# Optimization experiments

Hardware: AMD Instinct MI355X
Metric: run time of the kernel (lower is better)

The kernel has to match this reference:

```python
import jax, jax.numpy as jnp
import numpy as np

B, T, DIM, H, HD, K = 4, 2048, 1024, 16, 64, 4
QK = H * HD          # 1024
VD = 2 * H * HD      # 2048
EPS = 1e-5


def zrms(x, g):
    # zero-centered RMS norm with learned scale
    x = x - jnp.mean(x, axis=-1, keepdims=True)
    return x * jax.lax.rsqrt(jnp.mean(x * x, axis=-1, keepdims=True) + EPS) * g


def causal_dwconv(x, w):
    # x: [B,T,C], w: [K,1,C] (keras depthwise Conv1D kernel, groups=C)
    k = w.shape[0]
    return jax.lax.conv_general_dilated(
        x, w, window_strides=(1,), padding=[(k - 1, 0)],
        dimension_numbers=('NWC', 'WIO', 'NWC'),
        feature_group_count=x.shape[-1])


def setup_inputs() -> dict:
    key = jax.random.key(0)
    ks = jax.random.split(key, 12)
    s = lambda *sh: 1.0 / np.sqrt(sh[0])
    return {
        'x':  jax.random.normal(ks[0], (B, T, DIM), jnp.float32),
        'Wq': jax.random.normal(ks[1], (DIM, QK), jnp.float32) * s(DIM),
        'Wk': jax.random.normal(ks[2], (DIM, QK), jnp.float32) * s(DIM),
        'Wv': jax.random.normal(ks[3], (DIM, VD), jnp.float32) * s(DIM),
        'gq': jnp.ones((QK,), jnp.float32),
        'gk': jnp.ones((QK,), jnp.float32),
        'gv': jnp.ones((VD,), jnp.float32),
        'cq': jax.random.normal(ks[4], (K, 1, QK), jnp.float32) * 0.5,
        'ck': jax.random.normal(ks[5], (K, 1, QK), jnp.float32) * 0.5,
        'cv': jax.random.normal(ks[6], (K, 1, VD), jnp.float32) * 0.5,
        'Wa': jax.random.normal(ks[7], (DIM, H), jnp.float32) * s(DIM),
        'Wb': jax.random.normal(ks[8], (DIM, H), jnp.float32) * s(DIM),
        'Wo': jax.random.normal(ks[9], (VD, DIM), jnp.float32) * s(VD),
        'Wg': jax.random.normal(ks[10], (DIM, DIM), jnp.float32) * s(DIM),
    }


def reference(x, Wq, Wk, Wv, gq, gk, gv, cq, ck, cv, Wa, Wb, Wo, Wg):
    # 1) projections  2) zero-centered RMSNorm  3) causal depthwise conv (+silu)
    q = jax.nn.silu(causal_dwconv(zrms(x @ Wq, gq), cq))   # [B,T,QK]
    k = jax.nn.silu(causal_dwconv(zrms(x @ Wk, gk), ck))   # [B,T,QK]
    v = jax.nn.silu(causal_dwconv(zrms(x @ Wv, gv), cv))   # [B,T,VD]

    q = q.reshape(B, T, H, HD)
    k = k.reshape(B, T, H, HD)
    v = v.reshape(B, T, H, 2 * HD)

    # 4) per-head gating params
    alpha = jax.nn.sigmoid(x @ Wa)  # [B,T,H]
    beta = jax.nn.sigmoid(x @ Wb)   # [B,T,H]

    # 5) gated delta-rule recurrence over time (state S: [B,H,2*HD,HD])
    def step(S, inp):
        qt, kt, vt, at, bt = inp  # [B,H,HD],[B,H,HD],[B,H,2HD],[B,H],[B,H]
        a = at[..., None, None]
        upd = S + bt[..., None, None] * jnp.einsum('bhv,bhk->bhvk', vt, kt)
        S = a * upd + (1.0 - a) * S
        o = jnp.einsum('bhvk,bhk->bhv', S, qt)  # Q_t readout
        return S, o

    S0 = jnp.zeros((B, H, 2 * HD, HD), x.dtype)
    xs = (q.transpose(1, 0, 2, 3), k.transpose(1, 0, 2, 3),
          v.transpose(1, 0, 2, 3), alpha.transpose(1, 0, 2),
          beta.transpose(1, 0, 2))
    _, o = jax.lax.scan(step, S0, xs)          # o: [T,B,H,2HD]
    o = o.transpose(1, 0, 2, 3).reshape(B, T, VD)

    # 6) output projection + sigmoid output gate
    proj = o @ Wo                              # [B,T,DIM]
    return jax.nn.sigmoid(proj @ Wg) * proj
```

## Files before the change

### kernel.cpp

```cpp
#include <hip/hip_runtime.h>
#include <hip/hip_bf16.h>
#include <math.h>

#define RTOT 8192
#define TSEQ 2048

typedef __attribute__((ext_vector_type(8))) short short8;
typedef __attribute__((ext_vector_type(4))) float f32x4;
typedef unsigned short u16;
typedef unsigned int u32;

union U16x8 { uint4 v; u16 s[8]; };

__device__ __forceinline__ float sigmoidf_(float x) { return 1.f / (1.f + expf(-x)); }
__device__ __forceinline__ float bf2f(u16 v) { u32 u = ((u32)v) << 16; float f; __builtin_memcpy(&f, &u, 4); return f; }
__device__ __forceinline__ u16 f2bf(float f) {
  u32 u; __builtin_memcpy(&u, &f, 4);
  u32 r = (u + 0x7FFFu + ((u >> 16) & 1u)) >> 16;
  return (u16)r;
}
__device__ __forceinline__ void split2(float x, u16& h, u16& l) {
  u16 hh = f2bf(x);
  float hf = bf2f(hh);
  h = hh; l = f2bf(x - hf);
}

typedef const void __attribute__((address_space(1))) gvoid_t;
typedef void __attribute__((address_space(3))) lvoid_t;
__device__ __forceinline__ void gload_lds16(const void* g, void* l) {
  __builtin_amdgcn_global_load_lds((gvoid_t*)g, (lvoid_t*)l, 16, 0, 0);
}

template<int EPI>
__global__ __launch_bounds__(256) void gemm_sp(const u16* __restrict__ Ah, const u16* __restrict__ Al,
                                               const u16* __restrict__ Bh, const u16* __restrict__ Bl,
                                               float* __restrict__ Cf, u16* __restrict__ Ph,
                                               u16* __restrict__ Pl, const float* __restrict__ Pin,
                                               int M, int N, int K) {
  __shared__ u16 Ash[128 * 32], Asl[128 * 32];
  __shared__ u16 Bsh[128 * 32], Bsl[128 * 32];
  const int tid = threadIdx.x;
  const int l = tid & 63, w = tid >> 6;
  const int m0 = blockIdx.y * 128, n0 = blockIdx.x * 128;
  const int wr = w >> 1, wc = w & 1;
  f32x4 acc[4][4] = {};
  const int srow = (w << 5) + (l >> 2);
  const int scol = (l & 3) << 3;
  const size_t gA = (size_t)(m0 + srow) * K + scol;
  const size_t gB = (size_t)(n0 + srow) * K + scol;
  const int lo0 = (w * 2 + 0) * 512, lo1 = (w * 2 + 1) * 512;
  const int arow = wr * 64 + (l & 15), brow = wc * 64 + (l & 15);
  const int koff = 8 * (l >> 4);
  for (int k0 = 0; k0 < K; k0 += 32) {
    gload_lds16(Ah + gA + k0, &Ash[lo0]);
    gload_lds16(Ah + gA + 16 * K + k0, &Ash[lo1]);
    gload_lds16(Al + gA + k0, &Asl[lo0]);
    gload_lds16(Al + gA + 16 * K + k0, &Asl[lo1]);
    gload_lds16(Bh + gB + k0, &Bsh[lo0]);
    gload_lds16(Bh + gB + 16 * K + k0, &Bsh[lo1]);
    gload_lds16(Bl + gB + k0, &Bsl[lo0]);
    gload_lds16(Bl + gB + 16 * K + k0, &Bsl[lo1]);
    __syncthreads();
    short8 afh[4], afl[4], bfh[4], bfl[4];
#pragma unroll
    for (int m = 0; m < 4; ++m) {
      afh[m] = *(const short8*)&Ash[(arow + m * 16) * 32 + koff];
      afl[m] = *(const short8*)&Asl[(arow + m * 16) * 32 + koff];
    }
#pragma unroll
    for (int n = 0; n < 4; ++n) {
      bfh[n] = *(const short8*)&Bsh[(brow + n * 16) * 32 + koff];
      bfl[n] = *(const short8*)&Bsl[(brow + n * 16) * 32 + koff];
    }
#pragma unroll
    for (int m = 0; m < 4; ++m)
#pragma unroll
      for (int n = 0; n < 4; ++n) {
        acc[m][n] = __builtin_amdgcn_mfma_f32_16x16x32_bf16(afh[m], bfh[n], acc[m][n], 0, 0, 0);
        acc[m][n] = __builtin_amdgcn_mfma_f32_16x16x32_bf16(afh[m], bfl[n], acc[m][n], 0, 0, 0);
        acc[m][n] = __builtin_amdgcn_mfma_f32_16x16x32_bf16(afl[m], bfh[n], acc[m][n], 0, 0, 0);
      }
    __syncthreads();
  }
  const int rbase = m0 + wr * 64 + 4 * (l >> 4);
  const int cbase = n0 + wc * 64 + (l & 15);
#pragma unroll
  for (int m = 0; m < 4; ++m)
#pragma unroll
    for (int n = 0; n < 4; ++n)
#pragma unroll
      for (int r = 0; r < 4; ++r) {
        size_t idx = (size_t)(rbase + m * 16 + r) * N + (cbase + n * 16);
        float v = acc[m][n][r];
        if (EPI == 0) {
          Cf[idx] = v;
        } else if (EPI == 1) {
          Cf[idx] = v;
          u16 h, lo; split2(v, h, lo);
          Ph[idx] = h; Pl[idx] = lo;
        } else {
          Cf[idx] = Pin[idx] * sigmoidf_(v);
        }
      }
}

__global__ __launch_bounds__(256) void transcast_sp(const float* __restrict__ W,
                                                    u16* __restrict__ Wth, u16* __restrict__ Wtl,
                                                    int K, int N) {
  __shared__ float t[32][33];
  const int n0 = blockIdx.x * 32, k0 = blockIdx.y * 32;
  const int c = threadIdx.x & 31, rq = threadIdx.x >> 5;
#pragma unroll
  for (int i = 0; i < 4; ++i) t[rq * 4 + i][c] = W[(size_t)(k0 + rq * 4 + i) * N + n0 + c];
  __syncthreads();
#pragma unroll
  for (int i = 0; i < 4; ++i) {
    float v = t[c][rq * 4 + i];
    u16 h, lo; split2(v, h, lo);
    size_t idx = (size_t)(n0 + rq * 4 + i) * K + k0 + c;
    Wth[idx] = h; Wtl[idx] = lo;
  }
}

__global__ __launch_bounds__(256) void castx_sp(const float* __restrict__ x,
                                                u16* __restrict__ xh, u16* __restrict__ xl) {
  size_t i = (size_t)blockIdx.x * 256 + threadIdx.x;
  float4 v = ((const float4*)x)[i];
  ushort4 hh, ll;
  split2(v.x, hh.x, ll.x); split2(v.y, hh.y, ll.y);
  split2(v.z, hh.z, ll.z); split2(v.w, hh.w, ll.w);
  ((ushort4*)xh)[i] = hh; ((ushort4*)xl)[i] = ll;
}

template<int C>
__global__ __launch_bounds__(256) void zrms_kernel(const float* __restrict__ in,
                                                   const float* __restrict__ g,
                                                   float* __restrict__ out) {
  constexpr int NQ = C / 1024;
  __shared__ float red[4];
  const int tid = threadIdx.x;
  const size_t row = blockIdx.x;
  const float* x = in + row * C;
  float4 v[NQ];
  float s = 0.f;
#pragma unroll
  for (int i = 0; i < NQ; ++i) {
    v[i] = *(const float4*)(x + tid*4 + i*1024);
    s += v[i].x + v[i].y + v[i].z + v[i].w;
  }
#pragma unroll
  for (int o = 32; o > 0; o >>= 1) s += __shfl_xor(s, o, 64);
  if ((tid & 63) == 0) red[tid >> 6] = s;
  __syncthreads();
  const float mean = (red[0]+red[1]+red[2]+red[3]) * (1.f / C);
  __syncthreads();
  float ss = 0.f;
#pragma unroll
  for (int i = 0; i < NQ; ++i) {
    v[i].x -= mean; v[i].y -= mean; v[i].z -= mean; v[i].w -= mean;
    ss += v[i].x*v[i].x + v[i].y*v[i].y + v[i].z*v[i].z + v[i].w*v[i].w;
  }
#pragma unroll
  for (int o = 32; o > 0; o >>= 1) ss += __shfl_xor(ss, o, 64);
  if ((tid & 63) == 0) red[tid >> 6] = ss;
  __syncthreads();
  const float r = rsqrtf((red[0]+red[1]+red[2]+red[3]) * (1.f / C) + 1e-5f);
  float* y = out + row * C;
#pragma unroll
  for (int i = 0; i < NQ; ++i) {
    float4 g4 = *(const float4*)(g + tid*4 + i*1024);
    float4 o4;
    o4.x = v[i].x * r * g4.x;
    o4.y = v[i].y * r * g4.y;
    o4.z = v[i].z * r * g4.z;
    o4.w = v[i].w * r * g4.w;
    *(float4*)(y + tid*4 + i*1024) = o4;
  }
}

template<int C, int GSCALE>
__global__ __launch_bounds__(256) void conv_sp(const float* __restrict__ zn,
                                               const float* __restrict__ w,
                                               const float* __restrict__ g,
                                               u16* __restrict__ oh,
                                               u16* __restrict__ ol) {
  const size_t idx = (size_t)blockIdx.x * 256 + threadIdx.x;
  const int c = (int)(idx % (C/4)) * 4;
  const int row = (int)(idx / (C/4));
  const int t = row % TSEQ;
  float4 acc = {0.f, 0.f, 0.f, 0.f};
#pragma unroll
  for (int d = 0; d < 4; ++d) {
    if (t - d >= 0) {
      float4 xv = *(const float4*)(zn + (size_t)(row - d) * C + c);
      float4 wv = *(const float4*)(w + (size_t)(3 - d) * C + c);
      acc.x = fmaf(xv.x, wv.x, acc.x);
      acc.y = fmaf(xv.y, wv.y, acc.y);
      acc.z = fmaf(xv.z, wv.z, acc.z);
      acc.w = fmaf(xv.w, wv.w, acc.w);
    }
  }
  float a0 = acc.x * sigmoidf_(acc.x);
  float a1 = acc.y * sigmoidf_(acc.y);
  float a2 = acc.z * sigmoidf_(acc.z);
  float a3 = acc.w * sigmoidf_(acc.w);
  if (GSCALE) {
    float gv = g[(size_t)row * 16 + (c >> 7)];
    a0 *= gv; a1 *= gv; a2 *= gv; a3 *= gv;
  }
  ushort4 hh, ll;
  split2(a0, hh.x, ll.x); split2(a1, hh.y, ll.y);
  split2(a2, hh.z, ll.z); split2(a3, hh.w, ll.w);
  *(ushort4*)(oh + (size_t)row * C + c) = hh;
  *(ushort4*)(ol + (size_t)row * C + c) = ll;
}

__global__ __launch_bounds__(256) void gab_kernel(const float* __restrict__ x,
                                                  const float* __restrict__ Wa,
                                                  const float* __restrict__ Wb,
                                                  float* __restrict__ gout) {
  __shared__ float xs[1024];
  __shared__ float partial[256];
  const int tid = threadIdx.x;
  const size_t row = blockIdx.x;
  *(float4*)(&xs[tid*4]) = *(const float4*)(x + row*1024 + tid*4);
  __syncthreads();
  const int h = tid & 31;
  const int seg = tid >> 5;
  const float* W = (h < 16) ? Wa : Wb;
  const int col = h & 15;
  float s = 0.f;
  const int k0 = seg * 128;
  for (int k = 0; k < 128; ++k) s = fmaf(xs[k0 + k], W[(size_t)(k0 + k) * 16 + col], s);
  partial[tid] = s;
  __syncthreads();
  if (tid < 32) {
    float t2 = 0.f;
#pragma unroll
    for (int j = 0; j < 8; ++j) t2 += partial[j*32 + tid];
    partial[tid] = t2;
  }
  __syncthreads();
  if (tid < 16)
    gout[row*16 + tid] = sigmoidf_(partial[tid]) * sigmoidf_(partial[tid + 16]);
}

__global__ __launch_bounds__(256) void scan_kernel(const u16* __restrict__ kh,
                                                   const u16* __restrict__ kl,
                                                   const u16* __restrict__ vgh,
                                                   const u16* __restrict__ vgl,
                                                   u16* __restrict__ Sph,
                                                   u16* __restrict__ Spl) {
  __shared__ float Ks[64][68];
  __shared__ float Vs[64][36];
  const int tid = threadIdx.x;
  const int bid = blockIdx.x;
  const int vq = bid & 3, h = (bid >> 2) & 15, b = bid >> 6;
  const size_t rb = (size_t)b * TSEQ;
  const int vd_t = tid >> 3, kd0 = (tid & 7) * 8;
  float S[8] = {};
  const int sr = tid >> 2;
  const int kc0 = (tid & 3) * 16;
  const int vc0 = (tid & 3) * 8;
  for (int c = 0; c < 32; ++c) {
    {
      size_t off = (rb + (size_t)c * 64 + sr) * 1024 + h * 64 + kc0;
      U16x8 a0, a1, b0, b1;
      a0.v = *(const uint4*)(kh + off);     a1.v = *(const uint4*)(kh + off + 8);
      b0.v = *(const uint4*)(kl + off);     b1.v = *(const uint4*)(kl + off + 8);
#pragma unroll
      for (int j = 0; j < 8; ++j) {
        Ks[sr][kc0 + j]     = bf2f(a0.s[j]) + bf2f(b0.s[j]);
        Ks[sr][kc0 + 8 + j] = bf2f(a1.s[j]) + bf2f(b1.s[j]);
      }
      size_t voff = (rb + (size_t)c * 64 + sr) * 2048 + h * 128 + vq * 32 + vc0;
      U16x8 va, vb;
      va.v = *(const uint4*)(vgh + voff);   vb.v = *(const uint4*)(vgl + voff);
#pragma unroll
      for (int j = 0; j < 8; ++j) Vs[sr][vc0 + j] = bf2f(va.s[j]) + bf2f(vb.s[j]);
    }
    {
      size_t spc = (((size_t)(b * 16 + h) * 32) + c) * 8192 + (size_t)(vq * 32 + vd_t) * 64 + kd0;
      ushort4 h0, h1, l0, l1;
      split2(S[0], h0.x, l0.x); split2(S[1], h0.y, l0.y);
      split2(S[2], h0.z, l0.z); split2(S[3], h0.w, l0.w);
      split2(S[4], h1.x, l1.x); split2(S[5], h1.y, l1.y);
      split2(S[6], h1.z, l1.z); split2(S[7], h1.w, l1.w);
      *(ushort4*)(Sph + spc)     = h0;  *(ushort4*)(Sph + spc + 4) = h1;
      *(ushort4*)(Spl + spc)     = l0;  *(ushort4*)(Spl + spc + 4) = l1;
    }
    __syncthreads();
    for (int s = 0; s < 64; ++s) {
      float vv = Vs[s][vd_t];
      float k0v[4], k1v[4];
      *(float4*)k0v = *(const float4*)&Ks[s][kd0];
      *(float4*)k1v = *(const float4*)&Ks[s][kd0 + 4];
#pragma unroll
      for (int j = 0; j < 4; ++j) S[j] = fmaf(vv, k0v[j], S[j]);
#pragma unroll
      for (int j = 0; j < 4; ++j) S[4 + j] = fmaf(vv, k1v[j], S[4 + j]);
    }
    __syncthreads();
  }
}

__global__ __launch_bounds__(256) void pass2_sp(const u16* __restrict__ qh,
                                                const u16* __restrict__ ql,
                                                const u16* __restrict__ kh,
                                                const u16* __restrict__ vgh,
                                                const u16* __restrict__ Sph,
                                                const u16* __restrict__ Spl,
                                                u16* __restrict__ oh,
                                                u16* __restrict__ ol) {
  __shared__ u16 Qsh[64 * 72];
  __shared__ u16 Qsl[64 * 72];
  __shared__ u16 Ksm[64 * 72];
  __shared__ u16 Am[64 * 72];
  __shared__ u16 Vth[128 * 72];
  const int tid = threadIdx.x;
  const int l = tid & 63, w = tid >> 6;
  const int bid = blockIdx.x;
  const int c = bid & 31, h = (bid >> 5) & 15, b = bid >> 9;
  const size_t rb = (size_t)b * TSEQ + c * 64;
  const int fr = l & 15, fq = l >> 4;
  {
    int r = tid >> 2, c0 = (tid & 3) * 16;
    size_t off = (rb + r) * 1024 + h * 64 + c0;
    *(uint4*)&Qsh[r * 72 + c0]     = *(const uint4*)(qh + off);
    *(uint4*)&Qsh[r * 72 + c0 + 8] = *(const uint4*)(qh + off + 8);
    *(uint4*)&Qsl[r * 72 + c0]     = *(const uint4*)(ql + off);
    *(uint4*)&Qsl[r * 72 + c0 + 8] = *(const uint4*)(ql + off + 8);
    *(uint4*)&Ksm[r * 72 + c0]     = *(const uint4*)(kh + off);
    *(uint4*)&Ksm[r * 72 + c0 + 8] = *(const uint4*)(kh + off + 8);
  }
  {
    int s = tid >> 2, vd0 = (tid & 3) * 32;
    size_t off = (rb + s) * 2048 + h * 128 + vd0;
#pragma unroll
    for (int m4 = 0; m4 < 4; ++m4) {
      U16x8 r_; r_.v = *(const uint4*)(vgh + off + m4 * 8);
#pragma unroll
      for (int j = 0; j < 8; ++j) Vth[(vd0 + m4 * 8 + j) * 72 + s] = r_.s[j];
    }
  }
  __syncthreads();
  short8 aqh[2], aql[2];
#pragma unroll
  for (int kk = 0; kk < 2; ++kk) {
    aqh[kk] = *(const short8*)&Qsh[(w * 16 + fr) * 72 + kk * 32 + 8 * fq];
    aql[kk] = *(const short8*)&Qsl[(w * 16 + fr) * 72 + kk * 32 + 8 * fq];
  }
  f32x4 accA[4] = {};
#pragma unroll
  for (int n = 0; n < 4; ++n)
#pragma unroll
    for (int kk = 0; kk < 2; ++kk) {
      short8 bk = *(const short8*)&Ksm[(n * 16 + fr) * 72 + kk * 32 + 8 * fq];
      accA[n] = __builtin_amdgcn_mfma_f32_16x16x32_bf16(aqh[kk], bk, accA[n], 0, 0, 0);
    }
#pragma unroll
  for (int n = 0; n < 4; ++n)
#pragma unroll
    for (int rr = 0; rr < 4; ++rr) {
      int tt = w * 16 + 4 * fq + rr;
      int s = n * 16 + fr;
      Am[tt * 72 + s] = f2bf((s <= tt) ? accA[n][rr] : 0.f);
    }
  __syncthreads();
  f32x4 acc[8] = {};
#pragma unroll
  for (int kk = 0; kk < 2; ++kk) {
    short8 aa = *(const short8*)&Am[(w * 16 + fr) * 72 + kk * 32 + 8 * fq];
#pragma unroll
    for (int n = 0; n < 8; ++n) {
      short8 bv = *(const short8*)&Vth[(n * 16 + fr) * 72 + kk * 32 + 8 * fq];
      acc[n] = __builtin_amdgcn_mfma_f32_16x16x32_bf16(aa, bv, acc[n], 0, 0, 0);
    }
  }
  const size_t spb = (((size_t)(b * 16 + h) * 32) + c) * 8192;
#pragma unroll
  for (int n = 0; n < 8; ++n)
#pragma unroll
    for (int kk = 0; kk < 2; ++kk) {
      size_t soff = spb + (size_t)(n * 16 + fr) * 64 + kk * 32 + 8 * fq;
      short8 bh_ = *(const short8*)(Sph + soff);
      short8 bl_ = *(const short8*)(Spl + soff);
      acc[n] = __builtin_amdgcn_mfma_f32_16x16x32_bf16(aqh[kk], bh_, acc[n], 0, 0, 0);
      acc[n] = __builtin_amdgcn_mfma_f32_16x16x32_bf16(aqh[kk], bl_, acc[n], 0, 0, 0);
      acc[n] = __builtin_amdgcn_mfma_f32_16x16x32_bf16(aql[kk], bh_, acc[n], 0, 0, 0);
    }
#pragma unroll
  for (int n = 0; n < 8; ++n)
#pragma unroll
    for (int rr = 0; rr < 4; ++rr) {
      int tt = w * 16 + 4 * fq + rr;
      int vd = n * 16 + fr;
      u16 hh, ll;
      split2(acc[n][rr], hh, ll);
      size_t off = (rb + tt) * 2048 + h * 128 + vd;
      oh[off] = hh; ol[off] = ll;
    }
}

extern "C" void kernel_launch(void* const* d_in, const int* in_sizes, int n_in,
                              void* d_out, int out_size, void* d_ws, size_t ws_size,
                              hipStream_t stream) {
  (void)in_sizes; (void)n_in; (void)out_size; (void)ws_size;
  const float* x  = (const float*)d_in[0];
  const float* Wq = (const float*)d_in[1];
  const float* Wk = (const float*)d_in[2];
  const float* Wv = (const float*)d_in[3];
  const float* gq = (const float*)d_in[4];
  const float* gk = (const float*)d_in[5];
  const float* gv = (const float*)d_in[6];
  const float* cq = (const float*)d_in[7];
  const float* ck = (const float*)d_in[8];
  const float* cv = (const float*)d_in[9];
  const float* Wa = (const float*)d_in[10];
  const float* Wb = (const float*)d_in[11];
  const float* Wo = (const float*)d_in[12];
  const float* Wg = (const float*)d_in[13];
  float* out = (float*)d_out;
  char* ws = (char*)d_ws;

  const size_t MiB = 1024 * 1024;
  u16* Wq_h = (u16*)(ws + 0 * MiB);
  u16* Wq_l = (u16*)(ws + 2 * MiB);
  u16* Wk_h = (u16*)(ws + 4 * MiB);
  u16* Wk_l = (u16*)(ws + 6 * MiB);
  u16* Wv_h = (u16*)(ws + 8 * MiB);
  u16* Wv_l = (u16*)(ws + 12 * MiB);
  u16* Wo_h = (u16*)(ws + 16 * MiB);
  u16* Wo_l = (u16*)(ws + 20 * MiB);
  u16* Wg_h = (u16*)(ws + 24 * MiB);
  u16* Wg_l = (u16*)(ws + 26 * MiB);
  float* gbuf  = (float*)(ws + 28 * MiB);
  u16* x_h  = (u16*)(ws + 32 * MiB);
  u16* x_l  = (u16*)(ws + 48 * MiB);
  float* q_pre = (float*)(ws + 64 * MiB);
  float* k_pre = (float*)(ws + 96 * MiB);
  float* v_pre = (float*)(ws + 128 * MiB);
  u16* q_h = (u16*)(ws + 32 * MiB);
  u16* q_l = (u16*)(ws + 48 * MiB);
  u16* k_h = (u16*)(ws + 64 * MiB);
  u16* k_l = (u16*)(ws + 80 * MiB);
  u16* vg_h = (u16*)(ws + 96 * MiB);
  u16* vg_l = (u16*)d_out;
  u16* Sp_h = (u16*)(ws + 128 * MiB);
  u16* Sp_l = (u16*)(ws + 160 * MiB);
  u16* o_h  = (u16*)(ws + 192 * MiB);
  u16* o_l  = (u16*)d_out;
  float* proj = (float*)(ws + 64 * MiB);
  u16* p_h  = (u16*)(ws + 96 * MiB);
  u16* p_l  = (u16*)(ws + 112 * MiB);

  dim3 blk(256);
  castx_sp<<<dim3(8192), blk, 0, stream>>>(x, x_h, x_l);
  transcast_sp<<<dim3(32, 32), blk, 0, stream>>>(Wq, Wq_h, Wq_l, 1024, 1024);
  transcast_sp<<<dim3(32, 32), blk, 0, stream>>>(Wk, Wk_h, Wk_l, 1024, 1024);
  transcast_sp<<<dim3(64, 32), blk, 0, stream>>>(Wv, Wv_h, Wv_l, 1024, 2048);
  transcast_sp<<<dim3(32, 64), blk, 0, stream>>>(Wo, Wo_h, Wo_l, 2048, 1024);
  transcast_sp<<<dim3(32, 32), blk, 0, stream>>>(Wg, Wg_h, Wg_l, 1024, 1024);
  gab_kernel<<<dim3(8192), blk, 0, stream>>>(x, Wa, Wb, gbuf);
  gemm_sp<0><<<dim3(8, 64), blk, 0, stream>>>(x_h, x_l, Wq_h, Wq_l, q_pre, nullptr, nullptr, nullptr, 8192, 1024, 1024);
  gemm_sp<0><<<dim3(8, 64), blk, 0, stream>>>(x_h, x_l, Wk_h, Wk_l, k_pre, nullptr, nullptr, nullptr, 8192, 1024, 1024);
  gemm_sp<0><<<dim3(16, 64), blk, 0, stream>>>(x_h, x_l, Wv_h, Wv_l, v_pre, nullptr, nullptr, nullptr, 8192, 2048, 1024);
  zrms_kernel<1024><<<dim3(8192), blk, 0, stream>>>(q_pre, gq, q_pre);
  zrms_kernel<1024><<<dim3(8192), blk, 0, stream>>>(k_pre, gk, k_pre);
  zrms_kernel<2048><<<dim3(8192), blk, 0, stream>>>(v_pre, gv, v_pre);
  conv_sp<1024, 0><<<dim3(8192), blk, 0, stream>>>(q_pre, cq, nullptr, q_h, q_l);
  conv_sp<1024, 0><<<dim3(8192), blk, 0, stream>>>(k_pre, ck, nullptr, k_h, k_l);
  conv_sp<2048, 1><<<dim3(16384), blk, 0, stream>>>(v_pre, cv, gbuf, vg_h, vg_l);
  scan_kernel<<<dim3(256), blk, 0, stream>>>(k_h, k_l, vg_h, vg_l, Sp_h, Sp_l);
  pass2_sp<<<dim3(2048), blk, 0, stream>>>(q_h, q_l, k_h, vg_h, Sp_h, Sp_l, o_h, o_l);
  gemm_sp<1><<<dim3(8, 64), blk, 0, stream>>>(o_h, o_l, Wo_h, Wo_l, proj, p_h, p_l, nullptr, 8192, 1024, 2048);
  gemm_sp<2><<<dim3(8, 64), blk, 0, stream>>>(p_h, p_l, Wg_h, Wg_l, out, nullptr, nullptr, proj, 8192, 1024, 1024);
}
```

Measured before the change: 763.5 us.

## Merge Q/K GEMMs, fold zrms into conv, XCD-swizzle GEMM, split scan

Concatenates the transposed Wq and Wk so one GEMM produces Q and K together into a 2048-wide buffer. Replaces the zrms normalize-and-write kernels with a stats-only kernel storing per-row mean and rstd; the conv kernel applies the normalization and gain on the fly, removing a full read/write pass over the pre-activations. Adds an XCD-aware block remap in the GEMM for better L2 locality. Splits the chunk scan across the K dimension to double its block count, trading some redundant V loads for more parallelism.

```diff
diff --git a/kernel.cpp b/kernel.cpp
--- a/kernel.cpp
+++ b/kernel.cpp
@@ -29,6 +29,14 @@
 typedef void __attribute__((address_space(3))) lvoid_t;
 __device__ __forceinline__ void gload_lds16(const void* g, void* l) {
   __builtin_amdgcn_global_load_lds((gvoid_t*)g, (lvoid_t*)l, 16, 0, 0);
+}
+
+__device__ __forceinline__ void xcd_remap(int& bx, int& by) {
+  int gx = gridDim.x, nwg = gx * gridDim.y;
+  int bid = blockIdx.y * gx + blockIdx.x;
+  int cpx = nwg >> 3;
+  int swz = (bid & 7) * cpx + (bid >> 3);
+  bx = swz % gx; by = swz / gx;
 }
 
 template<int EPI>
@@ -39,9 +47,10 @@
                                                int M, int N, int K) {
   __shared__ u16 Ash[128 * 32], Asl[128 * 32];
   __shared__ u16 Bsh[128 * 32], Bsl[128 * 32];
+  int bx, by; xcd_remap(bx, by);
   const int tid = threadIdx.x;
   const int l = tid & 63, w = tid >> 6;
-  const int m0 = blockIdx.y * 128, n0 = blockIdx.x * 128;
+  const int m0 = by * 128, n0 = bx * 128;
   const int wr = w >> 1, wc = w & 1;
   f32x4 acc[4][4] = {};
   const int srow = (w << 5) + (l >> 2);
@@ -133,14 +142,13 @@
 }
 
 template<int C>
-__global__ __launch_bounds__(256) void zrms_kernel(const float* __restrict__ in,
-                                                   const float* __restrict__ g,
-                                                   float* __restrict__ out) {
+__global__ __launch_bounds__(256) void stats_kernel(const float* __restrict__ base,
+                                                    float* __restrict__ st) {
   constexpr int NQ = C / 1024;
   __shared__ float red[4];
   const int tid = threadIdx.x;
   const size_t row = blockIdx.x;
-  const float* x = in + row * C;
+  const float* x = base + row * 2048;
   float4 v[NQ];
   float s = 0.f;
 #pragma unroll
@@ -157,47 +165,44 @@
   float ss = 0.f;
 #pragma unroll
   for (int i = 0; i < NQ; ++i) {
-    v[i].x -= mean; v[i].y -= mean; v[i].z -= mean; v[i].w -= mean;
-    ss += v[i].x*v[i].x + v[i].y*v[i].y + v[i].z*v[i].z + v[i].w*v[i].w;
+    float a = v[i].x - mean, b = v[i].y - mean, c = v[i].z - mean, d = v[i].w - mean;
+    ss += a*a + b*b + c*c + d*d;
   }
 #pragma unroll
   for (int o = 32; o > 0; o >>= 1) ss += __shfl_xor(ss, o, 64);
   if ((tid & 63) == 0) red[tid >> 6] = ss;
   __syncthreads();
-  const float r = rsqrtf((red[0]+red[1]+red[2]+red[3]) * (1.f / C) + 1e-5f);
-  float* y = out + row * C;
-#pragma unroll
-  for (int i = 0; i < NQ; ++i) {
-    float4 g4 = *(const float4*)(g + tid*4 + i*1024);
-    float4 o4;
-    o4.x = v[i].x * r * g4.x;
-    o4.y = v[i].y * r * g4.y;
-    o4.z = v[i].z * r * g4.z;
-    o4.w = v[i].w * r * g4.w;
-    *(float4*)(y + tid*4 + i*1024) = o4;
+  if (tid == 0) {
+    st[row * 2] = mean;
+    st[row * 2 + 1] = rsqrtf((red[0]+red[1]+red[2]+red[3]) * (1.f / C) + 1e-5f);
   }
 }
 
 template<int C, int GSCALE>
-__global__ __launch_bounds__(256) void conv_sp(const float* __restrict__ zn,
+__global__ __launch_bounds__(256) void conv_ns(const float* __restrict__ zn,
+                                               const float* __restrict__ st,
                                                const float* __restrict__ w,
                                                const float* __restrict__ g,
+                                               const float* __restrict__ gab,
                                                u16* __restrict__ oh,
                                                u16* __restrict__ ol) {
   const size_t idx = (size_t)blockIdx.x * 256 + threadIdx.x;
   const int c = (int)(idx % (C/4)) * 4;
   const int row = (int)(idx / (C/4));
   const int t = row % TSEQ;
+  float4 g4 = *(const float4*)(g + c);
   float4 acc = {0.f, 0.f, 0.f, 0.f};
 #pragma unroll
   for (int d = 0; d < 4; ++d) {
     if (t - d >= 0) {
-      float4 xv = *(const float4*)(zn + (size_t)(row - d) * C + c);
+      const int r2 = row - d;
+      const float mean = st[r2 * 2], rstd = st[r2 * 2 + 1];
+      float4 xv = *(const float4*)(zn + (size_t)r2 * 2048 + c);
       float4 wv = *(const float4*)(w + (size_t)(3 - d) * C + c);
-      acc.x = fmaf(xv.x, wv.x, acc.x);
-      acc.y = fmaf(xv.y, wv.y, acc.y);
-      acc.z = fmaf(xv.z, wv.z, acc.z);
-      acc.w = fmaf(xv.w, wv.w, acc.w);
+      acc.x = fmaf((xv.x - mean) * rstd * g4.x, wv.x, acc.x);
+      acc.y = fmaf((xv.y - mean) * rstd * g4.y, wv.y, acc.y);
+      acc.z = fmaf((xv.z - mean) * rstd * g4.z, wv.z, acc.z);
+      acc.w = fmaf((xv.w - mean) * rstd * g4.w, wv.w, acc.w);
     }
   }
   float a0 = acc.x * sigmoidf_(acc.x);
@@ -205,7 +210,7 @@
   float a2 = acc.z * sigmoidf_(acc.z);
   float a3 = acc.w * sigmoidf_(acc.w);
   if (GSCALE) {
-    float gv = g[(size_t)row * 16 + (c >> 7)];
+    float gv = gab[(size_t)row * 16 + (c >> 7)];
     a0 *= gv; a1 *= gv; a2 *= gv; a3 *= gv;
   }
   ushort4 hh, ll;
@@ -251,54 +256,47 @@
                                                    const u16* __restrict__ vgl,
                                                    u16* __restrict__ Sph,
                                                    u16* __restrict__ Spl) {
-  __shared__ float Ks[64][68];
+  __shared__ float Ks[64][36];
   __shared__ float Vs[64][36];
   const int tid = threadIdx.x;
   const int bid = blockIdx.x;
-  const int vq = bid & 3, h = (bid >> 2) & 15, b = bid >> 6;
+  const int kq = bid & 1, vq = (bid >> 1) & 3, h = (bid >> 3) & 15, b = bid >> 7;
   const size_t rb = (size_t)b * TSEQ;
-  const int vd_t = tid >> 3, kd0 = (tid & 7) * 8;
-  float S[8] = {};
+  const int vd_t = tid >> 3, kd0 = (tid & 7) * 4;
+  float S[4] = {};
   const int sr = tid >> 2;
-  const int kc0 = (tid & 3) * 16;
-  const int vc0 = (tid & 3) * 8;
+  const int cc0 = (tid & 3) * 8;
   for (int c = 0; c < 32; ++c) {
     {
-      size_t off = (rb + (size_t)c * 64 + sr) * 1024 + h * 64 + kc0;
-      U16x8 a0, a1, b0, b1;
-      a0.v = *(const uint4*)(kh + off);     a1.v = *(const uint4*)(kh + off + 8);
-      b0.v = *(const uint4*)(kl + off);     b1.v = *(const uint4*)(kl + off + 8);
-#pragma unroll
-      for (int j = 0; j < 8; ++j) {
-        Ks[sr][kc0 + j]     = bf2f(a0.s[j]) + bf2f(b0.s[j]);
-        Ks[sr][kc0 + 8 + j] = bf2f(a1.s[j]) + bf2f(b1.s[j]);
-      }
-      size_t voff = (rb + (size_t)c * 64 + sr) * 2048 + h * 128 + vq * 32 + vc0;
+      size_t koffg = (rb + (size_t)c * 64 + sr) * 1024 + h * 64 + kq * 32 + cc0;
+      U16x8 a0, b0;
+      a0.v = *(const uint4*)(kh + koffg);
+      b0.v = *(const uint4*)(kl + koffg);
+#pragma unroll
+      for (int j = 0; j < 8; ++j) Ks[sr][cc0 + j] = bf2f(a0.s[j]) + bf2f(b0.s[j]);
+      size_t voffg = (rb + (size_t)c * 64 + sr) * 2048 + h * 128 + vq * 32 + cc0;
       U16x8 va, vb;
-      va.v = *(const uint4*)(vgh + voff);   vb.v = *(const uint4*)(vgl + voff);
-#pragma unroll
-      for (int j = 0; j < 8; ++j) Vs[sr][vc0 + j] = bf2f(va.s[j]) + bf2f(vb.s[j]);
+      va.v = *(const uint4*)(vgh + voffg);
+      vb.v = *(const uint4*)(vgl + voffg);
+#pragma unroll
+      for (int j = 0; j < 8; ++j) Vs[sr][cc0 + j] = bf2f(va.s[j]) + bf2f(vb.s[j]);
     }
     {
-      size_t spc = (((size_t)(b * 16 + h) * 32) + c) * 8192 + (size_t)(vq * 32 + vd_t) * 64 + kd0;
-      ushort4 h0, h1, l0, l1;
+      size_t spc = (((size_t)(b * 16 + h) * 32) + c) * 8192
+                 + (size_t)(vq * 32 + vd_t) * 64 + kq * 32 + kd0;
+      ushort4 h0, l0;
       split2(S[0], h0.x, l0.x); split2(S[1], h0.y, l0.y);
       split2(S[2], h0.z, l0.z); split2(S[3], h0.w, l0.w);
-      split2(S[4], h1.x, l1.x); split2(S[5], h1.y, l1.y);
-      split2(S[6], h1.z, l1.z); split2(S[7], h1.w, l1.w);
-      *(ushort4*)(Sph + spc)     = h0;  *(ushort4*)(Sph + spc + 4) = h1;
-      *(ushort4*)(Spl + spc)     = l0;  *(ushort4*)(Spl + spc + 4) = l1;
+      *(ushort4*)(Sph + spc) = h0;
+      *(ushort4*)(Spl + spc) = l0;
     }
     __syncthreads();
     for (int s = 0; s < 64; ++s) {
       float vv = Vs[s][vd_t];
-      float k0v[4], k1v[4];
-      *(float4*)k0v = *(const float4*)&Ks[s][kd0];
-      *(float4*)k1v = *(const float4*)&Ks[s][kd0 + 4];
-#pragma unroll
-      for (int j = 0; j < 4; ++j) S[j] = fmaf(vv, k0v[j], S[j]);
-#pragma unroll
-      for (int j = 0; j < 4; ++j) S[4 + j] = fmaf(vv, k1v[j], S[4 + j]);
+      float kv[4];
+      *(float4*)kv = *(const float4*)&Ks[s][kd0];
+#pragma unroll
+      for (int j = 0; j < 4; ++j) S[j] = fmaf(vv, kv[j], S[j]);
     }
     __syncthreads();
   }
@@ -424,31 +422,31 @@
   char* ws = (char*)d_ws;
 
   const size_t MiB = 1024 * 1024;
-  u16* Wq_h = (u16*)(ws + 0 * MiB);
-  u16* Wq_l = (u16*)(ws + 2 * MiB);
-  u16* Wk_h = (u16*)(ws + 4 * MiB);
-  u16* Wk_l = (u16*)(ws + 6 * MiB);
-  u16* Wv_h = (u16*)(ws + 8 * MiB);
-  u16* Wv_l = (u16*)(ws + 12 * MiB);
-  u16* Wo_h = (u16*)(ws + 16 * MiB);
-  u16* Wo_l = (u16*)(ws + 20 * MiB);
-  u16* Wg_h = (u16*)(ws + 24 * MiB);
-  u16* Wg_l = (u16*)(ws + 26 * MiB);
-  float* gbuf  = (float*)(ws + 28 * MiB);
-  u16* x_h  = (u16*)(ws + 32 * MiB);
-  u16* x_l  = (u16*)(ws + 48 * MiB);
-  float* q_pre = (float*)(ws + 64 * MiB);
-  float* k_pre = (float*)(ws + 96 * MiB);
-  float* v_pre = (float*)(ws + 128 * MiB);
-  u16* q_h = (u16*)(ws + 32 * MiB);
-  u16* q_l = (u16*)(ws + 48 * MiB);
-  u16* k_h = (u16*)(ws + 64 * MiB);
-  u16* k_l = (u16*)(ws + 80 * MiB);
-  u16* vg_h = (u16*)(ws + 96 * MiB);
-  u16* vg_l = (u16*)d_out;
+  u16* Wqk_h = (u16*)(ws + 0 * MiB);
+  u16* Wqk_l = (u16*)(ws + 4 * MiB);
+  u16* Wv_h  = (u16*)(ws + 8 * MiB);
+  u16* Wv_l  = (u16*)(ws + 12 * MiB);
+  u16* Wo_h  = (u16*)(ws + 16 * MiB);
+  u16* Wo_l  = (u16*)(ws + 20 * MiB);
+  u16* Wg_h  = (u16*)(ws + 24 * MiB);
+  u16* Wg_l  = (u16*)(ws + 26 * MiB);
+  float* gbuf = (float*)(ws + 28 * MiB);
+  float* st_q = (float*)(ws + 28 * MiB + 524288);
+  float* st_k = (float*)(ws + 28 * MiB + 524288 + 65536);
+  float* st_v = (float*)(ws + 28 * MiB + 524288 + 131072);
+  u16* x_h   = (u16*)(ws + 32 * MiB);
+  u16* x_l   = (u16*)(ws + 48 * MiB);
+  float* qk  = (float*)(ws + 64 * MiB);
+  float* vbuf = (float*)(ws + 128 * MiB);
+  u16* q_h = (u16*)(ws + 192 * MiB);
+  u16* q_l = (u16*)(ws + 208 * MiB);
+  u16* k_h = (u16*)(ws + 224 * MiB);
+  u16* k_l = (u16*)(ws + 240 * MiB);
+  u16* vg_h = (u16*)(ws + 64 * MiB);
+  u16* vg_l = (u16*)(ws + 96 * MiB);
   u16* Sp_h = (u16*)(ws + 128 * MiB);
   u16* Sp_l = (u16*)(ws + 160 * MiB);
-  u16* o_h  = (u16*)(ws + 192 * MiB);
+  u16* o_h  = (u16*)(ws + 32 * MiB);
   u16* o_l  = (u16*)d_out;
   float* proj = (float*)(ws + 64 * MiB);
   u16* p_h  = (u16*)(ws + 96 * MiB);
@@ -456,22 +454,21 @@
 
   dim3 blk(256);
   castx_sp<<<dim3(8192), blk, 0, stream>>>(x, x_h, x_l);
-  transcast_sp<<<dim3(32, 32), blk, 0, stream>>>(Wq, Wq_h, Wq_l, 1024, 1024);
-  transcast_sp<<<dim3(32, 32), blk, 0, stream>>>(Wk, Wk_h, Wk_l, 1024, 1024);
+  transcast_sp<<<dim3(32, 32), blk, 0, stream>>>(Wq, Wqk_h, Wqk_l, 1024, 1024);
+  transcast_sp<<<dim3(32, 32), blk, 0, stream>>>(Wk, Wqk_h + 1024 * 1024, Wqk_l + 1024 * 1024, 1024, 1024);
   transcast_sp<<<dim3(64, 32), blk, 0, stream>>>(Wv, Wv_h, Wv_l, 1024, 2048);
   transcast_sp<<<dim3(32, 64), blk, 0, stream>>>(Wo, Wo_h, Wo_l, 2048, 1024);
   transcast_sp<<<dim3(32, 32), blk, 0, stream>>>(Wg, Wg_h, Wg_l, 1024, 1024);
   gab_kernel<<<dim3(8192), blk, 0, stream>>>(x, Wa, Wb, gbuf);
-  gemm_sp<0><<<dim3(8, 64), blk, 0, stream>>>(x_h, x_l, Wq_h, Wq_l, q_pre, nullptr, nullptr, nullptr, 8192, 1024, 1024);
-  gemm_sp<0><<<dim3(8, 64), blk, 0, stream>>>(x_h, x_l, Wk_h, Wk_l, k_pre, nullptr, nullptr, nullptr, 8192, 1024, 1024);
-  gemm_sp<0><<<dim3(16, 64), blk, 0, stream>>>(x_h, x_l, Wv_h, Wv_l, v_pre, nullptr, nullptr, nullptr, 8192, 2048, 1024);
-  zrms_kernel<1024><<<dim3(8192), blk, 0, stream>>>(q_pre, gq, q_pre);
-  zrms_kernel<1024><<<dim3(8192), blk, 0, stream>>>(k_pre, gk, k_pre);
-  zrms_kernel<2048><<<dim3(8192), blk, 0, stream>>>(v_pre, gv, v_pre);
-  conv_sp<1024, 0><<<dim3(8192), blk, 0, stream>>>(q_pre, cq, nullptr, q_h, q_l);
-  conv_sp<1024, 0><<<dim3(8192), blk, 0, stream>>>(k_pre, ck, nullptr, k_h, k_l);
-  conv_sp<2048, 1><<<dim3(16384), blk, 0, stream>>>(v_pre, cv, gbuf, vg_h, vg_l);
-  scan_kernel<<<dim3(256), blk, 0, stream>>>(k_h, k_l, vg_h, vg_l, Sp_h, Sp_l);
+  gemm_sp<0><<<dim3(16, 64), blk, 0, stream>>>(x_h, x_l, Wqk_h, Wqk_l, qk, nullptr, nullptr, nullptr, 8192, 2048, 1024);
+  gemm_sp<0><<<dim3(16, 64), blk, 0, stream>>>(x_h, x_l, Wv_h, Wv_l, vbuf, nullptr, nullptr, nullptr, 8192, 2048, 1024);
+  stats_kernel<1024><<<dim3(8192), blk, 0, stream>>>(qk, st_q);
+  stats_kernel<1024><<<dim3(8192), blk, 0, stream>>>(qk + 1024, st_k);
+  stats_kernel<2048><<<dim3(8192), blk, 0, stream>>>(vbuf, st_v);
+  conv_ns<1024, 0><<<dim3(8192), blk, 0, stream>>>(qk, st_q, cq, gq, nullptr, q_h, q_l);
+  conv_ns<1024, 0><<<dim3(8192), blk, 0, stream>>>(qk + 1024, st_k, ck, gk, nullptr, k_h, k_l);
+  conv_ns<2048, 1><<<dim3(16384), blk, 0, stream>>>(vbuf, st_v, cv, gv, gbuf, vg_h, vg_l);
+  scan_kernel<<<dim3(512), blk, 0, stream>>>(k_h, k_l, vg_h, vg_l, Sp_h, Sp_l);
   pass2_sp<<<dim3(2048), blk, 0, stream>>>(q_h, q_l, k_h, vg_h, Sp_h, Sp_l, o_h, o_l);
   gemm_sp<1><<<dim3(8, 64), blk, 0, stream>>>(o_h, o_l, Wo_h, Wo_l, proj, p_h, p_l, nullptr, 8192, 1024, 2048);
   gemm_sp<2><<<dim3(8, 64), blk, 0, stream>>>(p_h, p_l, Wg_h, Wg_l, out, nullptr, nullptr, proj, 8192, 1024, 1024);
```

New measurement: 745.4 us. 2.4% less time.
